# Performance work log

Hardware: AMD Instinct MI355X
Metric: run time of the kernel (lower is better)

The kernel has to match this reference:

```python
import jax, jax.numpy as jnp
import numpy as np

B, S, D = 2, 2048, 1024
H = 16
HD = D // H
MINUS_INFINITY = -1000000000.0


def setup_inputs() -> dict:
    key = jax.random.key(0)
    ks = jax.random.split(key, 6)
    sc = 0.02
    return {
        "x": jax.random.normal(ks[0], (B, S, D), dtype=jnp.float32),
        "Wq": jax.random.normal(ks[1], (D, D), dtype=jnp.float32) * sc,
        "Wk": jax.random.normal(ks[2], (D, D), dtype=jnp.float32) * sc,
        "Wv": jax.random.normal(ks[3], (D, D), dtype=jnp.float32) * sc,
        "Wo": jax.random.normal(ks[4], (D, D), dtype=jnp.float32) * sc,
        "bo": jnp.zeros((D,), dtype=jnp.float32),
    }


def reference(x, Wq, Wk, Wv, Wo, bo):
    b, n, _ = x.shape
    # Linear with transpose_b=True: x @ W.T
    q = jnp.einsum('bnd,ed->bne', x, Wq).reshape(b, n, H, HD).transpose(0, 2, 1, 3)
    k = jnp.einsum('bnd,ed->bne', x, Wk).reshape(b, n, H, HD).transpose(0, 2, 1, 3)
    v = jnp.einsum('bnd,ed->bne', x, Wv).reshape(b, n, H, HD).transpose(0, 2, 1, 3)
    scores = jnp.einsum('bhqd,bhkd->bhqk', q, k) * (1.0 / HD ** 0.5)
    mask = jnp.triu(jnp.ones((n, n), dtype=scores.dtype), k=1) * MINUS_INFINITY
    scores = scores + mask[None, None, :, :]
    attn = jax.nn.softmax(scores, axis=-1)  # dropout prob = 0.0
    ctx = jnp.einsum('bhqk,bhkd->bhqd', attn, v)
    ctx = ctx.transpose(0, 2, 1, 3).reshape(b, n, D)
    return jnp.einsum('bnd,ed->bne', ctx, Wo) + bo
```

## Files before the change

kernel.cpp:

```cpp
#include <hip/hip_runtime.h>
#include <hip/hip_bf16.h>

#define B_  2
#define S_  2048
#define D_  1024
#define H_  16
#define HD_ 64

typedef __attribute__((ext_vector_type(8))) short short8;
typedef __attribute__((ext_vector_type(4))) float f32x4;

__device__ __forceinline__ unsigned short f2b(float f) {
    __hip_bfloat16 h = __float2bfloat16(f);
    unsigned short u;
    __builtin_memcpy(&u, &h, 2);
    return u;
}

__global__ __launch_bounds__(256) void convert_kernel(
    const float* __restrict__ x,  const float* __restrict__ Wq,
    const float* __restrict__ Wk, const float* __restrict__ Wv,
    const float* __restrict__ Wo, unsigned short* __restrict__ dst)
{
    const long long i4 = blockIdx.x * 256 + threadIdx.x;
    const long long e  = i4 * 4;
    const long long M1 = 1048576LL;
    const float* src;
    if      (e < 4 * M1) src = x  + e;
    else if (e < 5 * M1) src = Wq + (e - 4 * M1);
    else if (e < 6 * M1) src = Wk + (e - 5 * M1);
    else if (e < 7 * M1) src = Wv + (e - 6 * M1);
    else                 src = Wo + (e - 7 * M1);
    float4 v = *(const float4*)src;
    unsigned long long pk = (unsigned long long)f2b(v.x)
                          | ((unsigned long long)f2b(v.y) << 16)
                          | ((unsigned long long)f2b(v.z) << 32)
                          | ((unsigned long long)f2b(v.w) << 48);
    *(unsigned long long*)&dst[e] = pk;
}

__global__ __launch_bounds__(256) void qkv_proj_kernel(
    const unsigned short* __restrict__ x,
    const unsigned short* __restrict__ Wq,
    const unsigned short* __restrict__ Wk,
    const unsigned short* __restrict__ Wv,
    unsigned short* __restrict__ q_ws,
    unsigned short* __restrict__ k_ws,
    unsigned short* __restrict__ vT_ws)
{
    __shared__ unsigned short a_lds[128][72];
    __shared__ unsigned short b_lds[128][72];

    const int m0 = blockIdx.x * 128;
    const int n0 = blockIdx.y * 128;
    const int which = blockIdx.z;
    const unsigned short* W = (which == 0) ? Wq : (which == 1) ? Wk : Wv;

    const int tid  = threadIdx.x;
    const int wave = tid >> 6;
    const int lane = tid & 63;
    const int l15  = lane & 15;
    const int quad = lane >> 4;
    const int wm = (wave & 1) * 64;
    const int wn = (wave >> 1) * 64;

    f32x4 acc[4][4];
    #pragma unroll
    for (int sm = 0; sm < 4; ++sm)
        #pragma unroll
        for (int sn = 0; sn < 4; ++sn)
            #pragma unroll
            for (int r = 0; r < 4; ++r) acc[sm][sn][r] = 0.f;

    const int row = tid >> 3;
    const int c8  = tid & 7;

    for (int kk = 0; kk < D_; kk += 64) {
        #pragma unroll
        for (int rp = 0; rp < 4; ++rp) {
            *(uint4*)&a_lds[row + rp * 32][c8 * 8] =
                *(const uint4*)&x[(m0 + row + rp * 32) * D_ + kk + c8 * 8];
            *(uint4*)&b_lds[row + rp * 32][c8 * 8] =
                *(const uint4*)&W[(n0 + row + rp * 32) * D_ + kk + c8 * 8];
        }
        __syncthreads();
        #pragma unroll
        for (int kc = 0; kc < 2; ++kc) {
            short8 af[4], bf[4];
            #pragma unroll
            for (int s = 0; s < 4; ++s) {
                af[s] = *(const short8*)&a_lds[wm + s * 16 + l15][kc * 32 + quad * 8];
                bf[s] = *(const short8*)&b_lds[wn + s * 16 + l15][kc * 32 + quad * 8];
            }
            #pragma unroll
            for (int sm = 0; sm < 4; ++sm)
                #pragma unroll
                for (int sn = 0; sn < 4; ++sn)
                    acc[sm][sn] = __builtin_amdgcn_mfma_f32_16x16x32_bf16(
                        af[sm], bf[sn], acc[sm][sn], 0, 0, 0);
        }
        __syncthreads();
    }

    #pragma unroll
    for (int sm = 0; sm < 4; ++sm) {
        #pragma unroll
        for (int sn = 0; sn < 4; ++sn) {
            const int n  = n0 + wn + sn * 16 + l15;
            const int h  = n >> 6;
            const int hd = n & 63;
            const int mbase = m0 + wm + sm * 16 + quad * 4;
            const int b     = mbase >> 11;
            const int sbase = mbase & 2047;
            if (which == 2) {
                unsigned long long pk = 0;
                #pragma unroll
                for (int r = 0; r < 4; ++r)
                    pk |= (unsigned long long)f2b(acc[sm][sn][r]) << (16 * r);
                *(unsigned long long*)&vT_ws[((b * H_ + h) * HD_ + hd) * S_ + sbase] = pk;
            } else if (which == 0) {
                #pragma unroll
                for (int r = 0; r < 4; ++r)
                    q_ws[((b * H_ + h) * S_ + (sbase + r)) * HD_ + hd] =
                        f2b(acc[sm][sn][r] * 0.125f);
            } else {
                #pragma unroll
                for (int r = 0; r < 4; ++r)
                    k_ws[((b * H_ + h) * S_ + (sbase + r)) * HD_ + hd] =
                        f2b(acc[sm][sn][r]);
            }
        }
    }
}

__global__ __launch_bounds__(256) void attn_kernel(
    const unsigned short* __restrict__ q_ws,
    const unsigned short* __restrict__ k_ws,
    const unsigned short* __restrict__ vT_ws,
    unsigned short* __restrict__ ctx_ws)
{
    __shared__ unsigned short k_lds[2][64][72];
    __shared__ unsigned short vT_lds[2][64][72];

    const int pair = blockIdx.x;
    const int bh   = blockIdx.y;

    const int tid  = threadIdx.x;
    const int wave = tid >> 6;
    const int lane = tid & 63;
    const int l15  = lane & 15;
    const int quad = lane >> 4;
    const int row  = tid >> 3;
    const int c8   = tid & 7;

    const unsigned short* Qh = q_ws + bh * (S_ * HD_);
    const unsigned short* Kh = k_ws + bh * (S_ * HD_);
    const unsigned short* Vt = vT_ws + bh * (HD_ * S_);
    const int b = bh >> 4;
    const int h = bh & 15;

    const int src0 = l15 + 32 * (quad & 1);
    const int src1 = src0 + 16;
    const int sel  = quad >> 1;

    #pragma unroll
    for (int ph = 0; ph < 2; ++ph) {
        const int qt = (ph == 0) ? (31 - pair) : pair;
        const int q0 = qt * 64;
        const int qg = q0 + wave * 16 + l15;

        __syncthreads();
        *(uint4*)&k_lds[0][row][c8 * 8]       = *(const uint4*)&Kh[row * HD_ + c8 * 8];
        *(uint4*)&k_lds[0][row + 32][c8 * 8]  = *(const uint4*)&Kh[(row + 32) * HD_ + c8 * 8];
        *(uint4*)&vT_lds[0][row][c8 * 8]      = *(const uint4*)&Vt[row * S_ + c8 * 8];
        *(uint4*)&vT_lds[0][row + 32][c8 * 8] = *(const uint4*)&Vt[(row + 32) * S_ + c8 * 8];

        short8 aq[2];
        aq[0] = *(const short8*)&Qh[qg * HD_ + quad * 8];
        aq[1] = *(const short8*)&Qh[qg * HD_ + 32 + quad * 8];

        __syncthreads();

        float l_lane = 0.f;
        f32x4 o[4];
        #pragma unroll
        for (int f = 0; f < 4; ++f)
            #pragma unroll
            for (int r = 0; r < 4; ++r) o[f][r] = 0.f;

        for (int kt = 0; kt <= qt; ++kt) {
            const int cur = kt & 1;
            if (kt < qt) {
                const int nk0 = (kt + 1) * 64;
                const int nb  = cur ^ 1;
                *(uint4*)&k_lds[nb][row][c8 * 8]       = *(const uint4*)&Kh[(nk0 + row) * HD_ + c8 * 8];
                *(uint4*)&k_lds[nb][row + 32][c8 * 8]  = *(const uint4*)&Kh[(nk0 + row + 32) * HD_ + c8 * 8];
                *(uint4*)&vT_lds[nb][row][c8 * 8]      = *(const uint4*)&Vt[row * S_ + nk0 + c8 * 8];
                *(uint4*)&vT_lds[nb][row + 32][c8 * 8] = *(const uint4*)&Vt[(row + 32) * S_ + nk0 + c8 * 8];
            }

            f32x4 sc[4];
            #pragma unroll
            for (int f = 0; f < 4; ++f)
                #pragma unroll
                for (int r = 0; r < 4; ++r) sc[f][r] = 0.f;
            #pragma unroll
            for (int f = 0; f < 4; ++f)
                #pragma unroll
                for (int kc = 0; kc < 2; ++kc) {
                    short8 ak = *(const short8*)&k_lds[cur][f * 16 + l15][kc * 32 + quad * 8];
                    sc[f] = __builtin_amdgcn_mfma_f32_16x16x32_bf16(ak, aq[kc], sc[f], 0, 0, 0);
                }

            float p[4][4];
            if (kt == qt) {
                const int kbase = kt * 64 + quad * 4;
                #pragma unroll
                for (int f = 0; f < 4; ++f)
                    #pragma unroll
                    for (int r = 0; r < 4; ++r) {
                        const float pv = __expf(sc[f][r]);
                        p[f][r] = (kbase + f * 16 + r > qg) ? 0.f : pv;
                        l_lane += p[f][r];
                    }
            } else {
                #pragma unroll
                for (int f = 0; f < 4; ++f)
                    #pragma unroll
                    for (int r = 0; r < 4; ++r) {
                        p[f][r] = __expf(sc[f][r]);
                        l_lane += p[f][r];
                    }
            }

            unsigned int pd[4][2];
            #pragma unroll
            for (int f = 0; f < 4; ++f) {
                pd[f][0] = (unsigned int)f2b(p[f][0]) | ((unsigned int)f2b(p[f][1]) << 16);
                pd[f][1] = (unsigned int)f2b(p[f][2]) | ((unsigned int)f2b(p[f][3]) << 16);
            }

            #pragma unroll
            for (int c = 0; c < 2; ++c) {
                const int a0 = __shfl((int)pd[c * 2][0],     src0, 64);
                const int a1 = __shfl((int)pd[c * 2][1],     src0, 64);
                const int a2 = __shfl((int)pd[c * 2][0],     src1, 64);
                const int a3 = __shfl((int)pd[c * 2][1],     src1, 64);
                const int b0 = __shfl((int)pd[c * 2 + 1][0], src0, 64);
                const int b1 = __shfl((int)pd[c * 2 + 1][1], src0, 64);
                const int b2 = __shfl((int)pd[c * 2 + 1][0], src1, 64);
                const int b3 = __shfl((int)pd[c * 2 + 1][1], src1, 64);
                union { int i[4]; short8 s; } u2;
                u2.i[0] = sel ? b0 : a0;
                u2.i[1] = sel ? b1 : a1;
                u2.i[2] = sel ? b2 : a2;
                u2.i[3] = sel ? b3 : a3;
                #pragma unroll
                for (int f = 0; f < 4; ++f) {
                    short8 av = *(const short8*)&vT_lds[cur][f * 16 + l15][c * 32 + quad * 8];
                    o[f] = __builtin_amdgcn_mfma_f32_16x16x32_bf16(av, u2.s, o[f], 0, 0, 0);
                }
            }

            __syncthreads();
        }

        float l = l_lane;
        l += __shfl_xor(l, 16, 64);
        l += __shfl_xor(l, 32, 64);
        const float inv_l = 1.0f / l;

        #pragma unroll
        for (int f = 0; f < 4; ++f) {
            unsigned long long pk = 0;
            #pragma unroll
            for (int r = 0; r < 4; ++r)
                pk |= (unsigned long long)f2b(o[f][r] * inv_l) << (16 * r);
            *(unsigned long long*)&ctx_ws[(b * S_ + qg) * D_ + h * 64 + f * 16 + quad * 4] = pk;
        }
    }
}

__global__ __launch_bounds__(256) void out_proj_kernel(
    const unsigned short* __restrict__ ctx,
    const unsigned short* __restrict__ Wo,
    const float* __restrict__ bo,
    float* __restrict__ out)
{
    __shared__ unsigned short a_lds[128][72];
    __shared__ unsigned short b_lds[128][72];

    const int m0 = blockIdx.x * 128;
    const int n0 = blockIdx.y * 128;

    const int tid  = threadIdx.x;
    const int wave = tid >> 6;
    const int lane = tid & 63;
    const int l15  = lane & 15;
    const int quad = lane >> 4;
    const int wm = (wave & 1) * 64;
    const int wn = (wave >> 1) * 64;

    f32x4 acc[4][4];
    #pragma unroll
    for (int sm = 0; sm < 4; ++sm)
        #pragma unroll
        for (int sn = 0; sn < 4; ++sn)
            #pragma unroll
            for (int r = 0; r < 4; ++r) acc[sm][sn][r] = 0.f;

    const int row = tid >> 3;
    const int c8  = tid & 7;

    for (int kk = 0; kk < D_; kk += 64) {
        #pragma unroll
        for (int rp = 0; rp < 4; ++rp) {
            *(uint4*)&a_lds[row + rp * 32][c8 * 8] =
                *(const uint4*)&ctx[(m0 + row + rp * 32) * D_ + kk + c8 * 8];
            *(uint4*)&b_lds[row + rp * 32][c8 * 8] =
                *(const uint4*)&Wo[(n0 + row + rp * 32) * D_ + kk + c8 * 8];
        }
        __syncthreads();
        #pragma unroll
        for (int kc = 0; kc < 2; ++kc) {
            short8 af[4], bf[4];
            #pragma unroll
            for (int s = 0; s < 4; ++s) {
                af[s] = *(const short8*)&a_lds[wm + s * 16 + l15][kc * 32 + quad * 8];
                bf[s] = *(const short8*)&b_lds[wn + s * 16 + l15][kc * 32 + quad * 8];
            }
            #pragma unroll
            for (int sm = 0; sm < 4; ++sm)
                #pragma unroll
                for (int sn = 0; sn < 4; ++sn)
                    acc[sm][sn] = __builtin_amdgcn_mfma_f32_16x16x32_bf16(
                        af[sm], bf[sn], acc[sm][sn], 0, 0, 0);
        }
        __syncthreads();
    }

    #pragma unroll
    for (int sm = 0; sm < 4; ++sm) {
        #pragma unroll
        for (int sn = 0; sn < 4; ++sn) {
            const int n = n0 + wn + sn * 16 + l15;
            const float bias = bo[n];
            const int mbase = m0 + wm + sm * 16 + quad * 4;
            #pragma unroll
            for (int r = 0; r < 4; ++r)
                out[(mbase + r) * D_ + n] = acc[sm][sn][r] + bias;
        }
    }
}

extern "C" void kernel_launch(void* const* d_in, const int* in_sizes, int n_in,
                              void* d_out, int out_size, void* d_ws, size_t ws_size,
                              hipStream_t stream) {
    const float* x  = (const float*)d_in[0];
    const float* Wq = (const float*)d_in[1];
    const float* Wk = (const float*)d_in[2];
    const float* Wv = (const float*)d_in[3];
    const float* Wo = (const float*)d_in[4];
    const float* bo = (const float*)d_in[5];
    float* out = (float*)d_out;

    const size_t M1 = 1048576;
    const size_t SZ = 4 * M1;

    unsigned short* xb  = (unsigned short*)d_ws;
    unsigned short* wqb = xb  + SZ;
    unsigned short* wkb = wqb + M1;
    unsigned short* wvb = wkb + M1;
    unsigned short* wob = wvb + M1;
    unsigned short* q_ws   = wob + M1;
    unsigned short* k_ws   = q_ws + SZ;
    unsigned short* vT_ws  = k_ws + SZ;
    unsigned short* ctx_ws = vT_ws + SZ;

    convert_kernel<<<dim3(8192), 256, 0, stream>>>(x, Wq, Wk, Wv, Wo, xb);
    qkv_proj_kernel<<<dim3(32, 8, 3), 256, 0, stream>>>(xb, wqb, wkb, wvb, q_ws, k_ws, vT_ws);
    attn_kernel<<<dim3(16, 32), 256, 0, stream>>>(q_ws, k_ws, vT_ws, ctx_ws);
    out_proj_kernel<<<dim3(32, 8), 256, 0, stream>>>(ctx_ws, wob, bo, out);
}
```

Before: 190.3 us.

## Use direct global-to-LDS loads in GEMMs and split attention into one tile per block

The QKV and output projection GEMMs now fill shared memory with global_load_lds (16-byte direct global-to-LDS DMA) into an unpadded 64-wide layout, which skips the staging of tiles through registers. The attention kernel no longer pairs a long and a short query tile in each block. It launches one block per query tile (32x32 grid), heaviest tiles first. Removing the LDS padding may add bank conflicts on the MFMA fragment reads, and the new grid loses the built-in load balancing that pairing gave.

```diff
diff --git a/kernel.cpp b/kernel.cpp
--- a/kernel.cpp
+++ b/kernel.cpp
@@ -15,6 +15,12 @@
     unsigned short u;
     __builtin_memcpy(&u, &h, 2);
     return u;
+}
+
+typedef __attribute__((address_space(1))) const unsigned int g_u32;
+typedef __attribute__((address_space(3))) unsigned int l_u32;
+__device__ __forceinline__ void gload_lds16(const void* g, void* l) {
+    __builtin_amdgcn_global_load_lds((g_u32*)g, (l_u32*)l, 16, 0, 0);
 }
 
 __global__ __launch_bounds__(256) void convert_kernel(
@@ -48,8 +54,8 @@
     unsigned short* __restrict__ k_ws,
     unsigned short* __restrict__ vT_ws)
 {
-    __shared__ unsigned short a_lds[128][72];
-    __shared__ unsigned short b_lds[128][72];
+    __shared__ unsigned short a_lds[128 * 64];
+    __shared__ unsigned short b_lds[128 * 64];
 
     const int m0 = blockIdx.x * 128;
     const int n0 = blockIdx.y * 128;
@@ -72,16 +78,14 @@
             #pragma unroll
             for (int r = 0; r < 4; ++r) acc[sm][sn][r] = 0.f;
 
-    const int row = tid >> 3;
-    const int c8  = tid & 7;
-
     for (int kk = 0; kk < D_; kk += 64) {
         #pragma unroll
-        for (int rp = 0; rp < 4; ++rp) {
-            *(uint4*)&a_lds[row + rp * 32][c8 * 8] =
-                *(const uint4*)&x[(m0 + row + rp * 32) * D_ + kk + c8 * 8];
-            *(uint4*)&b_lds[row + rp * 32][c8 * 8] =
-                *(const uint4*)&W[(n0 + row + rp * 32) * D_ + kk + c8 * 8];
+        for (int p = 0; p < 4; ++p) {
+            const int off = (p * 256 + tid) * 16;
+            const int r   = off >> 7;
+            const int cs  = (off & 127) >> 1;
+            gload_lds16(&x[(m0 + r) * D_ + kk + cs], &a_lds[off >> 1]);
+            gload_lds16(&W[(n0 + r) * D_ + kk + cs], &b_lds[off >> 1]);
         }
         __syncthreads();
         #pragma unroll
@@ -89,8 +93,8 @@
             short8 af[4], bf[4];
             #pragma unroll
             for (int s = 0; s < 4; ++s) {
-                af[s] = *(const short8*)&a_lds[wm + s * 16 + l15][kc * 32 + quad * 8];
-                bf[s] = *(const short8*)&b_lds[wn + s * 16 + l15][kc * 32 + quad * 8];
+                af[s] = *(const short8*)&a_lds[(wm + s * 16 + l15) * 64 + kc * 32 + quad * 8];
+                bf[s] = *(const short8*)&b_lds[(wn + s * 16 + l15) * 64 + kc * 32 + quad * 8];
             }
             #pragma unroll
             for (int sm = 0; sm < 4; ++sm)
@@ -142,8 +146,8 @@
     __shared__ unsigned short k_lds[2][64][72];
     __shared__ unsigned short vT_lds[2][64][72];
 
-    const int pair = blockIdx.x;
-    const int bh   = blockIdx.y;
+    const int bh = blockIdx.x;
+    const int qt = 31 - (int)blockIdx.y;
 
     const int tid  = threadIdx.x;
     const int wave = tid >> 6;
@@ -163,121 +167,116 @@
     const int src1 = src0 + 16;
     const int sel  = quad >> 1;
 
-    #pragma unroll
-    for (int ph = 0; ph < 2; ++ph) {
-        const int qt = (ph == 0) ? (31 - pair) : pair;
-        const int q0 = qt * 64;
-        const int qg = q0 + wave * 16 + l15;
-
-        __syncthreads();
-        *(uint4*)&k_lds[0][row][c8 * 8]       = *(const uint4*)&Kh[row * HD_ + c8 * 8];
-        *(uint4*)&k_lds[0][row + 32][c8 * 8]  = *(const uint4*)&Kh[(row + 32) * HD_ + c8 * 8];
-        *(uint4*)&vT_lds[0][row][c8 * 8]      = *(const uint4*)&Vt[row * S_ + c8 * 8];
-        *(uint4*)&vT_lds[0][row + 32][c8 * 8] = *(const uint4*)&Vt[(row + 32) * S_ + c8 * 8];
-
-        short8 aq[2];
-        aq[0] = *(const short8*)&Qh[qg * HD_ + quad * 8];
-        aq[1] = *(const short8*)&Qh[qg * HD_ + 32 + quad * 8];
-
-        __syncthreads();
-
-        float l_lane = 0.f;
-        f32x4 o[4];
+    const int q0 = qt * 64;
+    const int qg = q0 + wave * 16 + l15;
+
+    *(uint4*)&k_lds[0][row][c8 * 8]       = *(const uint4*)&Kh[row * HD_ + c8 * 8];
+    *(uint4*)&k_lds[0][row + 32][c8 * 8]  = *(const uint4*)&Kh[(row + 32) * HD_ + c8 * 8];
+    *(uint4*)&vT_lds[0][row][c8 * 8]      = *(const uint4*)&Vt[row * S_ + c8 * 8];
+    *(uint4*)&vT_lds[0][row + 32][c8 * 8] = *(const uint4*)&Vt[(row + 32) * S_ + c8 * 8];
+
+    short8 aq[2];
+    aq[0] = *(const short8*)&Qh[qg * HD_ + quad * 8];
+    aq[1] = *(const short8*)&Qh[qg * HD_ + 32 + quad * 8];
+
+    __syncthreads();
+
+    float l_lane = 0.f;
+    f32x4 o[4];
+    #pragma unroll
+    for (int f = 0; f < 4; ++f)
+        #pragma unroll
+        for (int r = 0; r < 4; ++r) o[f][r] = 0.f;
+
+    for (int kt = 0; kt <= qt; ++kt) {
+        const int cur = kt & 1;
+        if (kt < qt) {
+            const int nk0 = (kt + 1) * 64;
+            const int nb  = cur ^ 1;
+            *(uint4*)&k_lds[nb][row][c8 * 8]       = *(const uint4*)&Kh[(nk0 + row) * HD_ + c8 * 8];
+            *(uint4*)&k_lds[nb][row + 32][c8 * 8]  = *(const uint4*)&Kh[(nk0 + row + 32) * HD_ + c8 * 8];
+            *(uint4*)&vT_lds[nb][row][c8 * 8]      = *(const uint4*)&Vt[row * S_ + nk0 + c8 * 8];
+            *(uint4*)&vT_lds[nb][row + 32][c8 * 8] = *(const uint4*)&Vt[(row + 32) * S_ + nk0 + c8 * 8];
+        }
+
+        f32x4 sc[4];
         #pragma unroll
         for (int f = 0; f < 4; ++f)
             #pragma unroll
-            for (int r = 0; r < 4; ++r) o[f][r] = 0.f;
-
-        for (int kt = 0; kt <= qt; ++kt) {
-            const int cur = kt & 1;
-            if (kt < qt) {
-                const int nk0 = (kt + 1) * 64;
-                const int nb  = cur ^ 1;
-                *(uint4*)&k_lds[nb][row][c8 * 8]       = *(const uint4*)&Kh[(nk0 + row) * HD_ + c8 * 8];
-                *(uint4*)&k_lds[nb][row + 32][c8 * 8]  = *(const uint4*)&Kh[(nk0 + row + 32) * HD_ + c8 * 8];
-                *(uint4*)&vT_lds[nb][row][c8 * 8]      = *(const uint4*)&Vt[row * S_ + nk0 + c8 * 8];
-                *(uint4*)&vT_lds[nb][row + 32][c8 * 8] = *(const uint4*)&Vt[(row + 32) * S_ + nk0 + c8 * 8];
-            }
-
-            f32x4 sc[4];
+            for (int r = 0; r < 4; ++r) sc[f][r] = 0.f;
+        #pragma unroll
+        for (int f = 0; f < 4; ++f)
+            #pragma unroll
+            for (int kc = 0; kc < 2; ++kc) {
+                short8 ak = *(const short8*)&k_lds[cur][f * 16 + l15][kc * 32 + quad * 8];
+                sc[f] = __builtin_amdgcn_mfma_f32_16x16x32_bf16(ak, aq[kc], sc[f], 0, 0, 0);
+            }
+
+        float p[4][4];
+        if (kt == qt) {
+            const int kbase = kt * 64 + quad * 4;
             #pragma unroll
             for (int f = 0; f < 4; ++f)
                 #pragma unroll
-                for (int r = 0; r < 4; ++r) sc[f][r] = 0.f;
+                for (int r = 0; r < 4; ++r) {
+                    const float pv = __expf(sc[f][r]);
+                    p[f][r] = (kbase + f * 16 + r > qg) ? 0.f : pv;
+                    l_lane += p[f][r];
+                }
+        } else {
             #pragma unroll
             for (int f = 0; f < 4; ++f)
                 #pragma unroll
-                for (int kc = 0; kc < 2; ++kc) {
-                    short8 ak = *(const short8*)&k_lds[cur][f * 16 + l15][kc * 32 + quad * 8];
-                    sc[f] = __builtin_amdgcn_mfma_f32_16x16x32_bf16(ak, aq[kc], sc[f], 0, 0, 0);
+                for (int r = 0; r < 4; ++r) {
+                    p[f][r] = __expf(sc[f][r]);
+                    l_lane += p[f][r];
                 }
-
-            float p[4][4];
-            if (kt == qt) {
-                const int kbase = kt * 64 + quad * 4;
-                #pragma unroll
-                for (int f = 0; f < 4; ++f)
-                    #pragma unroll
-                    for (int r = 0; r < 4; ++r) {
-                        const float pv = __expf(sc[f][r]);
-                        p[f][r] = (kbase + f * 16 + r > qg) ? 0.f : pv;
-                        l_lane += p[f][r];
-                    }
-            } else {
-                #pragma unroll
-                for (int f = 0; f < 4; ++f)
-                    #pragma unroll
-                    for (int r = 0; r < 4; ++r) {
-                        p[f][r] = __expf(sc[f][r]);
-                        l_lane += p[f][r];
-                    }
-            }
-
-            unsigned int pd[4][2];
+        }
+
+        unsigned int pd[4][2];
+        #pragma unroll
+        for (int f = 0; f < 4; ++f) {
+            pd[f][0] = (unsigned int)f2b(p[f][0]) | ((unsigned int)f2b(p[f][1]) << 16);
+            pd[f][1] = (unsigned int)f2b(p[f][2]) | ((unsigned int)f2b(p[f][3]) << 16);
+        }
+
+        #pragma unroll
+        for (int c = 0; c < 2; ++c) {
+            const int a0 = __shfl((int)pd[c * 2][0],     src0, 64);
+            const int a1 = __shfl((int)pd[c * 2][1],     src0, 64);
+            const int a2 = __shfl((int)pd[c * 2][0],     src1, 64);
+            const int a3 = __shfl((int)pd[c * 2][1],     src1, 64);
+            const int b0 = __shfl((int)pd[c * 2 + 1][0], src0, 64);
+            const int b1 = __shfl((int)pd[c * 2 + 1][1], src0, 64);
+            const int b2 = __shfl((int)pd[c * 2 + 1][0], src1, 64);
+            const int b3 = __shfl((int)pd[c * 2 + 1][1], src1, 64);
+            union { int i[4]; short8 s; } u2;
+            u2.i[0] = sel ? b0 : a0;
+            u2.i[1] = sel ? b1 : a1;
+            u2.i[2] = sel ? b2 : a2;
+            u2.i[3] = sel ? b3 : a3;
             #pragma unroll
             for (int f = 0; f < 4; ++f) {
-                pd[f][0] = (unsigned int)f2b(p[f][0]) | ((unsigned int)f2b(p[f][1]) << 16);
-                pd[f][1] = (unsigned int)f2b(p[f][2]) | ((unsigned int)f2b(p[f][3]) << 16);
-            }
-
-            #pragma unroll
-            for (int c = 0; c < 2; ++c) {
-                const int a0 = __shfl((int)pd[c * 2][0],     src0, 64);
-                const int a1 = __shfl((int)pd[c * 2][1],     src0, 64);
-                const int a2 = __shfl((int)pd[c * 2][0],     src1, 64);
-                const int a3 = __shfl((int)pd[c * 2][1],     src1, 64);
-                const int b0 = __shfl((int)pd[c * 2 + 1][0], src0, 64);
-                const int b1 = __shfl((int)pd[c * 2 + 1][1], src0, 64);
-                const int b2 = __shfl((int)pd[c * 2 + 1][0], src1, 64);
-                const int b3 = __shfl((int)pd[c * 2 + 1][1], src1, 64);
-                union { int i[4]; short8 s; } u2;
-                u2.i[0] = sel ? b0 : a0;
-                u2.i[1] = sel ? b1 : a1;
-                u2.i[2] = sel ? b2 : a2;
-                u2.i[3] = sel ? b3 : a3;
-                #pragma unroll
-                for (int f = 0; f < 4; ++f) {
-                    short8 av = *(const short8*)&vT_lds[cur][f * 16 + l15][c * 32 + quad * 8];
-                    o[f] = __builtin_amdgcn_mfma_f32_16x16x32_bf16(av, u2.s, o[f], 0, 0, 0);
-                }
-            }
-
-            __syncthreads();
-        }
-
-        float l = l_lane;
-        l += __shfl_xor(l, 16, 64);
-        l += __shfl_xor(l, 32, 64);
-        const float inv_l = 1.0f / l;
-
-        #pragma unroll
-        for (int f = 0; f < 4; ++f) {
-            unsigned long long pk = 0;
-            #pragma unroll
-            for (int r = 0; r < 4; ++r)
-                pk |= (unsigned long long)f2b(o[f][r] * inv_l) << (16 * r);
-            *(unsigned long long*)&ctx_ws[(b * S_ + qg) * D_ + h * 64 + f * 16 + quad * 4] = pk;
-        }
+                short8 av = *(const short8*)&vT_lds[cur][f * 16 + l15][c * 32 + quad * 8];
+                o[f] = __builtin_amdgcn_mfma_f32_16x16x32_bf16(av, u2.s, o[f], 0, 0, 0);
+            }
+        }
+
+        __syncthreads();
+    }
+
+    float l = l_lane;
+    l += __shfl_xor(l, 16, 64);
+    l += __shfl_xor(l, 32, 64);
+    const float inv_l = 1.0f / l;
+
+    #pragma unroll
+    for (int f = 0; f < 4; ++f) {
+        unsigned long long pk = 0;
+        #pragma unroll
+        for (int r = 0; r < 4; ++r)
+            pk |= (unsigned long long)f2b(o[f][r] * inv_l) << (16 * r);
+        *(unsigned long long*)&ctx_ws[(b * S_ + qg) * D_ + h * 64 + f * 16 + quad * 4] = pk;
     }
 }
 
@@ -287,8 +286,8 @@
     const float* __restrict__ bo,
     float* __restrict__ out)
 {
-    __shared__ unsigned short a_lds[128][72];
-    __shared__ unsigned short b_lds[128][72];
+    __shared__ unsigned short a_lds[128 * 64];
+    __shared__ unsigned short b_lds[128 * 64];
 
     const int m0 = blockIdx.x * 128;
     const int n0 = blockIdx.y * 128;
@@ -309,16 +308,14 @@
             #pragma unroll
             for (int r = 0; r < 4; ++r) acc[sm][sn][r] = 0.f;
 
-    const int row = tid >> 3;
-    const int c8  = tid & 7;
-
     for (int kk = 0; kk < D_; kk += 64) {
         #pragma unroll
-        for (int rp = 0; rp < 4; ++rp) {
-            *(uint4*)&a_lds[row + rp * 32][c8 * 8] =
-                *(const uint4*)&ctx[(m0 + row + rp * 32) * D_ + kk + c8 * 8];
-            *(uint4*)&b_lds[row + rp * 32][c8 * 8] =
-                *(const uint4*)&Wo[(n0 + row + rp * 32) * D_ + kk + c8 * 8];
+        for (int p = 0; p < 4; ++p) {
+            const int off = (p * 256 + tid) * 16;
+            const int r   = off >> 7;
+            const int cs  = (off & 127) >> 1;
+            gload_lds16(&ctx[(m0 + r) * D_ + kk + cs], &a_lds[off >> 1]);
+            gload_lds16(&Wo[(n0 + r) * D_ + kk + cs],  &b_lds[off >> 1]);
         }
         __syncthreads();
         #pragma unroll
@@ -326,8 +323,8 @@
             short8 af[4], bf[4];
             #pragma unroll
             for (int s = 0; s < 4; ++s) {
-                af[s] = *(const short8*)&a_lds[wm + s * 16 + l15][kc * 32 + quad * 8];
-                bf[s] = *(const short8*)&b_lds[wn + s * 16 + l15][kc * 32 + quad * 8];
+                af[s] = *(const short8*)&a_lds[(wm + s * 16 + l15) * 64 + kc * 32 + quad * 8];
+                bf[s] = *(const short8*)&b_lds[(wn + s * 16 + l15) * 64 + kc * 32 + quad * 8];
             }
             #pragma unroll
             for (int sm = 0; sm < 4; ++sm)
@@ -379,6 +376,6 @@
 
     convert_kernel<<<dim3(8192), 256, 0, stream>>>(x, Wq, Wk, Wv, Wo, xb);
     qkv_proj_kernel<<<dim3(32, 8, 3), 256, 0, stream>>>(xb, wqb, wkb, wvb, q_ws, k_ws, vT_ws);
-    attn_kernel<<<dim3(16, 32), 256, 0, stream>>>(q_ws, k_ws, vT_ws, ctx_ws);
+    attn_kernel<<<dim3(32, 32), 256, 0, stream>>>(q_ws, k_ws, vT_ws, ctx_ws);
     out_proj_kernel<<<dim3(32, 8), 256, 0, stream>>>(ctx_ws, wob, bo, out);
 }
```

After: 203.7 us. 1.07x slower.
